# Kernel optimization log

Measured on AMD Instinct MI355X. Metric: run time of the kernel, lower is better.

The kernel has to match this reference:

```python
import jax, jax.numpy as jnp
import numpy as np

B = 262144      # batch (many robot-timestep samples)
IN_LEN = 32     # input_len
S = 64          # internal_state_len
M = 32          # message_len
P = 4           # num_ports
H = 100         # hidden_layer_size
L = 50          # lstm_hidden_size
O = 16          # output_len


def _linear_init(key, out_f, in_f):
    # torch.nn.Linear default init: U(-1/sqrt(in_f), 1/sqrt(in_f)) for W and b
    kw, kb = jax.random.split(key)
    bound = 1.0 / np.sqrt(in_f)
    W = jax.random.uniform(kw, (out_f, in_f), jnp.float32, -bound, bound)
    b = jax.random.uniform(kb, (out_f,), jnp.float32, -bound, bound)
    return W, b


def setup_inputs() -> dict:
    key = jax.random.key(0)
    ks = jax.random.split(key, 20)
    obs = jax.random.normal(ks[0], (B, IN_LEN), jnp.float32)
    messages_in = jax.random.normal(ks[1], (P, B, M), jnp.float32)
    h_lstm = jax.random.normal(ks[2], (B, L), jnp.float32)
    c_lstm = jax.random.normal(ks[3], (B, L), jnp.float32)

    W_in, b_in = _linear_init(ks[4], S, IN_LEN)
    # per-port message MLPs, stacked on a leading port axis
    msg1 = [_linear_init(jax.random.fold_in(ks[5], p), H, S) for p in range(P)]
    msg2 = [_linear_init(jax.random.fold_in(ks[6], p), M, H) for p in range(P)]
    msg_W1 = jnp.stack([w for w, _ in msg1])  # [P, H, S]
    msg_b1 = jnp.stack([b for _, b in msg1])  # [P, H]
    msg_W2 = jnp.stack([w for w, _ in msg2])  # [P, M, H]
    msg_b2 = jnp.stack([b for _, b in msg2])  # [P, M]

    # LSTMCell(S + M*P -> L); torch gate order i, f, g, o; init U(-1/sqrt(L), 1/sqrt(L))
    bl = 1.0 / np.sqrt(L)
    W_ih = jax.random.uniform(ks[7], (4 * L, S + M * P), jnp.float32, -bl, bl)
    W_hh = jax.random.uniform(ks[8], (4 * L, L), jnp.float32, -bl, bl)
    b_ih = jax.random.uniform(ks[9], (4 * L,), jnp.float32, -bl, bl)
    b_hh = jax.random.uniform(ks[10], (4 * L,), jnp.float32, -bl, bl)

    W_u1, b_u1 = _linear_init(ks[11], H, L)
    W_u2, b_u2 = _linear_init(ks[12], H, H)
    W_u3, b_u3 = _linear_init(ks[13], S, H)
    W_mu, b_mu = _linear_init(ks[14], O, S)
    W_var, b_var = _linear_init(ks[15], O, S)
    max_logvar = jnp.ones((1, O), jnp.float32) / 2.0
    min_logvar = -jnp.ones((1, O), jnp.float32) * 10.0

    return dict(obs=obs, messages_in=messages_in, h_lstm=h_lstm, c_lstm=c_lstm,
                W_in=W_in, b_in=b_in, msg_W1=msg_W1, msg_b1=msg_b1,
                msg_W2=msg_W2, msg_b2=msg_b2, W_ih=W_ih, W_hh=W_hh,
                b_ih=b_ih, b_hh=b_hh, W_u1=W_u1, b_u1=b_u1, W_u2=W_u2,
                b_u2=b_u2, W_u3=W_u3, b_u3=b_u3, W_mu=W_mu, b_mu=b_mu,
                W_var=W_var, b_var=b_var, max_logvar=max_logvar,
                min_logvar=min_logvar)


def reference(obs, messages_in, h_lstm, c_lstm, W_in, b_in, msg_W1, msg_b1,
              msg_W2, msg_b2, W_ih, W_hh, b_ih, b_hh, W_u1, b_u1, W_u2, b_u2,
              W_u3, b_u3, W_mu, b_mu, W_var, b_var, max_logvar, min_logvar):
    # run_input_function
    x = jax.nn.relu(obs @ W_in.T + b_in)                       # [B, S]

    # compute_messages_out_function: batched over ports (all ports occupied)
    m1 = jax.nn.relu(jnp.einsum('bs,phs->pbh', x, msg_W1) + msg_b1[:, None, :])
    msgs_out = jnp.einsum('pbh,pmh->pbm', m1, msg_W2) + msg_b2[:, None, :]  # [P, B, M]

    # compute_aggregation_function: concat incoming messages along feature dim
    agg = jnp.transpose(messages_in, (1, 0, 2)).reshape(obs.shape[0], -1)  # [B, P*M]
    h_mbar = jnp.concatenate([x, agg], axis=-1)                # [B, S + P*M]

    # status_update_function: one LSTMCell step (torch gate order i, f, g, o)
    gates = h_mbar @ W_ih.T + b_ih + h_lstm @ W_hh.T + b_hh    # [B, 4L]
    i, f, g, o = jnp.split(gates, 4, axis=-1)
    c_new = jax.nn.sigmoid(f) * c_lstm + jax.nn.sigmoid(i) * jnp.tanh(g)
    h_new = jax.nn.sigmoid(o) * jnp.tanh(c_new)                # [B, L]
    h2 = jax.nn.relu(h_new @ W_u1.T + b_u1)
    h2 = jax.nn.relu(h2 @ W_u2.T + b_u2)
    h2 = h2 @ W_u3.T + b_u3                                    # new internal state [B, S]

    # compute_output_function with soft logvar clamping
    mu = h2 @ W_mu.T + b_mu                                    # [B, O]
    logvar = h2 @ W_var.T + b_var
    logvar = max_logvar - jax.nn.softplus(max_logvar - logvar)
    logvar = min_logvar + jax.nn.softplus(logvar - min_logvar)
    var = jnp.exp(logvar)

    msgs_flat = jnp.transpose(msgs_out, (1, 0, 2)).reshape(obs.shape[0], -1)  # [B, P*M]
    # concat all outputs: mu(16) var(16) msgs(128) h2(64) h_new(50) c_new(50) = 324
    return jnp.concatenate([mu, var, msgs_flat, h2, h_new, c_new], axis=-1)
```

## Files before the change

### kernel.cpp

```cpp
#include <hip/hip_runtime.h>

typedef __bf16 bf16_t;
typedef __bf16 bf16x8 __attribute__((ext_vector_type(8)));
typedef float f32x4 __attribute__((ext_vector_type(4)));

#define B_TOTAL 262144
#define OUTC 324
#define ROWS 64

#define OFF_WIN   0
#define OFF_WG    2048
#define OFF_WM1   67584
#define OFF_WM2   96256
#define OFF_WU1   112640
#define OFF_WU2   119808
#define OFF_WU3   134144
#define OFF_WMV2  142336
#define BF16_TOTAL 145920

__global__ void prep_kernel(const float* W_in, const float* msg_W1, const float* msg_W2,
                            const float* W_ih, const float* W_hh, const float* b_ih, const float* b_hh,
                            const float* W_u1, const float* W_u2, const float* W_u3, const float* b_u3f,
                            const float* W_mu, const float* W_var, const float* b_mu, const float* b_var,
                            bf16_t* wb, float* bg, float* bmv) {
  int tid = blockIdx.x * blockDim.x + threadIdx.x;
  int nth = gridDim.x * blockDim.x;
  for (int i = tid; i < 2048; i += nth) wb[OFF_WIN + i] = (bf16_t)W_in[i];
  for (int i = tid; i < 65536; i += nth) {
    int n = i >> 8, k = i & 255;
    int g = n >> 6, j = n & 63;
    float v = 0.f;
    if (j < 50) {
      int r = g * 50 + j;
      if (k < 192) v = W_ih[r * 192 + k];
      else if (k < 242) v = W_hh[r * 50 + (k - 192)];
    }
    wb[OFF_WG + i] = (bf16_t)v;
  }
  for (int i = tid; i < 256; i += nth) {
    int g = i >> 6, j = i & 63;
    bg[i] = (j < 50) ? (b_ih[g * 50 + j] + b_hh[g * 50 + j]) : 0.f;
  }
  for (int i = tid; i < 4 * 112 * 64; i += nth) {
    int p = i / (112 * 64); int rem = i % (112 * 64); int n = rem >> 6, k = rem & 63;
    wb[OFF_WM1 + i] = (bf16_t)((n < 100) ? msg_W1[(p * 100 + n) * 64 + k] : 0.f);
  }
  for (int i = tid; i < 4 * 32 * 128; i += nth) {
    int p = i / (32 * 128); int rem = i % (32 * 128); int n = rem >> 7, k = rem & 127;
    wb[OFF_WM2 + i] = (bf16_t)((k < 100) ? msg_W2[(p * 32 + n) * 100 + k] : 0.f);
  }
  for (int i = tid; i < 112 * 64; i += nth) {
    int n = i >> 6, k = i & 63;
    wb[OFF_WU1 + i] = (bf16_t)((n < 100 && k < 50) ? W_u1[n * 50 + k] : 0.f);
  }
  for (int i = tid; i < 112 * 128; i += nth) {
    int n = i >> 7, k = i & 127;
    wb[OFF_WU2 + i] = (bf16_t)((n < 100 && k < 100) ? W_u2[n * 100 + k] : 0.f);
  }
  for (int i = tid; i < 64 * 128; i += nth) {
    int n = i >> 7, k = i & 127;
    wb[OFF_WU3 + i] = (bf16_t)((k < 100) ? W_u3[n * 100 + k] : 0.f);
  }
  for (int i = tid; i < 32 * 112; i += nth) {
    int o = i / 112, h = i % 112;
    float v = 0.f;
    if (h < 100) {
      const float* wrow = (o < 16) ? (W_mu + o * 64) : (W_var + (o - 16) * 64);
      for (int s = 0; s < 64; s++) v += wrow[s] * W_u3[s * 100 + h];
    }
    wb[OFF_WMV2 + i] = (bf16_t)v;
  }
  for (int i = tid; i < 32; i += nth) {
    int o = i;
    const float* wrow = (o < 16) ? (W_mu + o * 64) : (W_var + (o - 16) * 64);
    float v = (o < 16) ? b_mu[o] : b_var[o - 16];
    for (int s = 0; s < 64; s++) v += wrow[s] * b_u3f[s];
    bmv[o] = v;
  }
}

#define MFMA(a, b, c) __builtin_amdgcn_mfma_f32_16x16x32_bf16((a), (b), (c), 0, 0, 0)

__device__ __forceinline__ float frcp(float x) { return __builtin_amdgcn_rcpf(x); }
__device__ __forceinline__ float fsigmoid(float x) { return frcp(1.f + __expf(-x)); }
__device__ __forceinline__ float ftanh_f(float x) { return 1.f - 2.f * frcp(1.f + __expf(2.f * x)); }
__device__ __forceinline__ float fsoftplus(float x) { return (x > 15.f) ? x : __logf(1.f + __expf(x)); }

__device__ __forceinline__ bf16x8 cvt8(const float* __restrict__ p) {
  float4 v0 = *(const float4*)p;
  float4 v1 = *(const float4*)(p + 4);
  bf16x8 r;
  r[0] = (bf16_t)v0.x; r[1] = (bf16_t)v0.y; r[2] = (bf16_t)v0.z; r[3] = (bf16_t)v0.w;
  r[4] = (bf16_t)v1.x; r[5] = (bf16_t)v1.y; r[6] = (bf16_t)v1.z; r[7] = (bf16_t)v1.w;
  return r;
}

__device__ __forceinline__ void stage2(int p, const bf16x8 ax[4][2], bf16_t* dst,
                                       const bf16_t* __restrict__ wb,
                                       const float* __restrict__ msg_b1,
                                       int w, int lr, int kq) {
  for (int nt = w; nt < 7; nt += 4) {
    int nb = nt * 16;
    float bv = (nb + lr < 100) ? msg_b1[p * 100 + nb + lr] : 0.f;
    const bf16_t* Bp = wb + OFF_WM1 + p * 112 * 64 + (nb + lr) * 64 + kq * 8;
    bf16x8 b0 = *(const bf16x8*)Bp;
    bf16x8 b1 = *(const bf16x8*)(Bp + 32);
#pragma unroll
    for (int m = 0; m < 4; m++) {
      f32x4 acc = {bv, bv, bv, bv};
      acc = MFMA(ax[m][0], b0, acc);
      acc = MFMA(ax[m][1], b1, acc);
#pragma unroll
      for (int rr = 0; rr < 4; rr++)
        dst[(m * 16 + kq * 4 + rr) * 120 + nb + lr] = (bf16_t)fmaxf(acc[rr], 0.f);
    }
  }
}

__device__ __forceinline__ void stage3(int p, const bf16_t* src,
                                       const bf16_t* __restrict__ wb,
                                       const float* __restrict__ msg_b2,
                                       float* __restrict__ out,
                                       int row0, int w, int lr, int kq) {
  int nb = (w & 1) * 16;
  float bv = msg_b2[p * 32 + nb + lr];
  const bf16_t* Bp = wb + OFF_WM2 + p * 32 * 128 + (nb + lr) * 128 + kq * 8;
  bf16x8 b[4];
#pragma unroll
  for (int c = 0; c < 4; c++) b[c] = *(const bf16x8*)(Bp + c * 32);
#pragma unroll
  for (int mi = 0; mi < 2; mi++) {
    int m = (w >> 1) + mi * 2;
    f32x4 acc = {bv, bv, bv, bv};
#pragma unroll
    for (int c = 0; c < 4; c++) {
      bf16x8 a;
      if (c < 3) {
        a = *(const bf16x8*)(src + (m * 16 + lr) * 120 + c * 32 + kq * 8);
      } else {
        bf16x8 z = {};
        a = (kq < 2) ? *(const bf16x8*)(src + (m * 16 + lr) * 120 + 96 + kq * 8) : z;
      }
      acc = MFMA(a, b[c], acc);
    }
#pragma unroll
    for (int rr = 0; rr < 4; rr++) {
      size_t row = row0 + m * 16 + kq * 4 + rr;
      out[row * OUTC + 32 + p * 32 + nb + lr] = acc[rr];
    }
  }
}

__global__ __launch_bounds__(256, 2) void fused_kernel(
    const float* __restrict__ obs, const float* __restrict__ msg_in,
    const float* __restrict__ h_lstm, const float* __restrict__ c_lstm,
    const float* __restrict__ b_in, const float* __restrict__ msg_b1,
    const float* __restrict__ msg_b2, const float* __restrict__ b_u1,
    const float* __restrict__ b_u2, const float* __restrict__ b_u3,
    const float* __restrict__ maxlv, const float* __restrict__ minlv,
    const bf16_t* __restrict__ wb, const float* __restrict__ bg,
    const float* __restrict__ bmv, float* __restrict__ out) {
  __shared__ __align__(16) bf16_t xh[ROWS * 72];
  __shared__ __align__(16) bf16_t tA[ROWS * 120];
  __shared__ __align__(16) bf16_t tB[ROWS * 120];

  const int tid = threadIdx.x;
  const int row0 = blockIdx.x * ROWS;
  const int lane = tid & 63;
  const int w = tid >> 6;
  const int lr = lane & 15;
  const int kq = lane >> 4;

  {
    int nb = w * 16;
    float bv = b_in[nb + lr];
    bf16x8 b0 = *(const bf16x8*)(wb + OFF_WIN + (nb + lr) * 32 + kq * 8);
#pragma unroll
    for (int m = 0; m < 4; m++) {
      bf16x8 a0 = cvt8(obs + (size_t)(row0 + m * 16 + lr) * 32 + kq * 8);
      f32x4 acc = {bv, bv, bv, bv};
      acc = MFMA(a0, b0, acc);
#pragma unroll
      for (int rr = 0; rr < 4; rr++)
        xh[(m * 16 + kq * 4 + rr) * 72 + nb + lr] = (bf16_t)fmaxf(acc[rr], 0.f);
    }
  }
  __syncthreads();

  bf16x8 ax[4][2];
#pragma unroll
  for (int m = 0; m < 4; m++)
#pragma unroll
    for (int k = 0; k < 2; k++)
      ax[m][k] = *(const bf16x8*)(xh + (m * 16 + lr) * 72 + k * 32 + kq * 8);

  stage2(0, ax, tA, wb, msg_b1, w, lr, kq);
  __syncthreads();

  stage3(0, tA, wb, msg_b2, out, row0, w, lr, kq);
  stage2(1, ax, tB, wb, msg_b1, w, lr, kq);
  __syncthreads();
  stage3(1, tB, wb, msg_b2, out, row0, w, lr, kq);
  stage2(2, ax, tA, wb, msg_b1, w, lr, kq);
  __syncthreads();
  stage3(2, tA, wb, msg_b2, out, row0, w, lr, kq);
  stage2(3, ax, tB, wb, msg_b1, w, lr, kq);
  __syncthreads();

  {
    const int mt = w >> 1, jh = w & 1;
    const int jbase = jh * 32;
    bf16x8 m_pre[4][2];
#pragma unroll
    for (int p = 0; p < 4; p++)
#pragma unroll
      for (int ms = 0; ms < 2; ms++)
        m_pre[p][ms] = cvt8(msg_in + ((size_t)p * B_TOTAL + row0 + mt * 32 + ms * 16 + lr) * 32 + kq * 8);
    bf16x8 h_pre[2][2];
#pragma unroll
    for (int ms = 0; ms < 2; ms++) {
      const float* hp = h_lstm + (size_t)(row0 + mt * 32 + ms * 16 + lr) * 50;
      h_pre[0][ms] = cvt8(hp + kq * 8);
      if (kq < 2) {
        h_pre[1][ms] = cvt8(hp + 32 + kq * 8);
      } else if (kq == 2) {
        bf16x8 r = {};
        float2 v = *(const float2*)(hp + 48);
        r[0] = (bf16_t)v.x; r[1] = (bf16_t)v.y;
        h_pre[1][ms] = r;
      } else {
        bf16x8 r = {};
        h_pre[1][ms] = r;
      }
    }
    float c_pre[2][2][4];
#pragma unroll
    for (int s = 0; s < 2; s++) {
      int j = jbase + s * 16 + lr;
#pragma unroll
      for (int ms = 0; ms < 2; ms++)
#pragma unroll
        for (int rr = 0; rr < 4; rr++) {
          size_t row = row0 + mt * 32 + ms * 16 + kq * 4 + rr;
          c_pre[s][ms][rr] = (j < 50) ? c_lstm[row * 50 + j] : 0.f;
        }
    }

    stage3(3, tB, wb, msg_b2, out, row0, w, lr, kq);

    f32x4 acc[4][2][2];
#pragma unroll
    for (int g = 0; g < 4; g++)
#pragma unroll
      for (int s = 0; s < 2; s++) {
        float bb = bg[g * 64 + jbase + s * 16 + lr];
        f32x4 bi = {bb, bb, bb, bb};
        acc[g][s][0] = bi;
        acc[g][s][1] = bi;
      }
#pragma unroll
    for (int c = 0; c < 8; c++) {
      bf16x8 a[2];
#pragma unroll
      for (int ms = 0; ms < 2; ms++) {
        int lrow = mt * 32 + ms * 16 + lr;
        if (c < 2) {
          a[ms] = *(const bf16x8*)(xh + lrow * 72 + c * 32 + kq * 8);
        } else if (c < 6) {
          a[ms] = m_pre[c - 2][ms];
        } else {
          a[ms] = h_pre[c - 6][ms];
        }
      }
#pragma unroll
      for (int g = 0; g < 4; g++)
#pragma unroll
        for (int s = 0; s < 2; s++) {
          bf16x8 bfrag = *(const bf16x8*)(wb + OFF_WG +
              (size_t)(g * 64 + jbase + s * 16 + lr) * 256 + c * 32 + kq * 8);
          acc[g][s][0] = MFMA(a[0], bfrag, acc[g][s][0]);
          acc[g][s][1] = MFMA(a[1], bfrag, acc[g][s][1]);
        }
    }
#pragma unroll
    for (int s = 0; s < 2; s++) {
      int j = jbase + s * 16 + lr;
#pragma unroll
      for (int ms = 0; ms < 2; ms++) {
        int rbase = mt * 32 + ms * 16 + kq * 4;
#pragma unroll
        for (int rr = 0; rr < 4; rr++) {
          int lrow = rbase + rr;
          size_t row = row0 + lrow;
          float si = fsigmoid(acc[0][s][ms][rr]);
          float sf = fsigmoid(acc[1][s][ms][rr]);
          float gv = ftanh_f(acc[2][s][ms][rr]);
          float so = fsigmoid(acc[3][s][ms][rr]);
          float cn = sf * c_pre[s][ms][rr] + si * gv;
          float hv = so * ftanh_f(cn);
          if (j < 50) {
            out[row * OUTC + 274 + j] = cn;
            out[row * OUTC + 224 + j] = hv;
          }
          tA[lrow * 120 + j] = (bf16_t)((j < 50) ? hv : 0.f);
        }
      }
    }
  }
  __syncthreads();

  for (int nt = w; nt < 7; nt += 4) {
    int nb = nt * 16;
    float bv = (nb + lr < 100) ? b_u1[nb + lr] : 0.f;
    const bf16_t* Bp = wb + OFF_WU1 + (nb + lr) * 64 + kq * 8;
    bf16x8 b0 = *(const bf16x8*)Bp;
    bf16x8 b1 = *(const bf16x8*)(Bp + 32);
#pragma unroll
    for (int m = 0; m < 4; m++) {
      bf16x8 a0 = *(const bf16x8*)(tA + (m * 16 + lr) * 120 + kq * 8);
      bf16x8 a1 = *(const bf16x8*)(tA + (m * 16 + lr) * 120 + kq * 8 + 32);
      f32x4 acc = {bv, bv, bv, bv};
      acc = MFMA(a0, b0, acc);
      acc = MFMA(a1, b1, acc);
#pragma unroll
      for (int rr = 0; rr < 4; rr++)
        tB[(m * 16 + kq * 4 + rr) * 120 + nb + lr] = (bf16_t)fmaxf(acc[rr], 0.f);
    }
  }
  __syncthreads();

  for (int nt = w; nt < 7; nt += 4) {
    int nb = nt * 16;
    float bv = (nb + lr < 100) ? b_u2[nb + lr] : 0.f;
    const bf16_t* Bp = wb + OFF_WU2 + (nb + lr) * 128 + kq * 8;
    bf16x8 b[4];
#pragma unroll
    for (int c = 0; c < 4; c++) b[c] = *(const bf16x8*)(Bp + c * 32);
#pragma unroll
    for (int m = 0; m < 4; m++) {
      f32x4 acc = {bv, bv, bv, bv};
#pragma unroll
      for (int c = 0; c < 4; c++) {
        bf16x8 a;
        if (c < 3) {
          a = *(const bf16x8*)(tB + (m * 16 + lr) * 120 + c * 32 + kq * 8);
        } else {
          bf16x8 z = {};
          a = (kq < 2) ? *(const bf16x8*)(tB + (m * 16 + lr) * 120 + 96 + kq * 8) : z;
        }
        acc = MFMA(a, b[c], acc);
      }
#pragma unroll
      for (int rr = 0; rr < 4; rr++)
        tA[(m * 16 + kq * 4 + rr) * 120 + nb + lr] = (bf16_t)fmaxf(acc[rr], 0.f);
    }
  }
  __syncthreads();

  {
    int nb = w * 16;
    float bv = b_u3[nb + lr];
    const bf16_t* Bp = wb + OFF_WU3 + (nb + lr) * 128 + kq * 8;
    bf16x8 b[4];
#pragma unroll
    for (int c = 0; c < 4; c++) b[c] = *(const bf16x8*)(Bp + c * 32);
#pragma unroll
    for (int m = 0; m < 4; m++) {
      f32x4 acc = {bv, bv, bv, bv};
#pragma unroll
      for (int c = 0; c < 4; c++) {
        bf16x8 a;
        if (c < 3) {
          a = *(const bf16x8*)(tA + (m * 16 + lr) * 120 + c * 32 + kq * 8);
        } else {
          bf16x8 z = {};
          a = (kq < 2) ? *(const bf16x8*)(tA + (m * 16 + lr) * 120 + 96 + kq * 8) : z;
        }
        acc = MFMA(a, b[c], acc);
      }
#pragma unroll
      for (int rr = 0; rr < 4; rr++) {
        size_t row = row0 + m * 16 + kq * 4 + rr;
        out[row * OUTC + 160 + nb + lr] = acc[rr];
      }
    }
  }

  {
    int t = w & 1;
    const bf16_t* Bp = wb + OFF_WMV2 + (t * 16 + lr) * 112 + kq * 8;
    bf16x8 b[4];
#pragma unroll
    for (int c = 0; c < 3; c++) b[c] = *(const bf16x8*)(Bp + c * 32);
    {
      bf16x8 z = {};
      b[3] = (kq < 2) ? *(const bf16x8*)(Bp + 96) : z;
    }
    float bv = bmv[t * 16 + lr];
    float mx = maxlv[lr], mn = minlv[lr];
#pragma unroll
    for (int mi = 0; mi < 2; mi++) {
      int m = (w >> 1) + mi * 2;
      f32x4 acc = {bv, bv, bv, bv};
#pragma unroll
      for (int c = 0; c < 4; c++) {
        bf16x8 a;
        if (c < 3) {
          a = *(const bf16x8*)(tA + (m * 16 + lr) * 120 + c * 32 + kq * 8);
        } else {
          bf16x8 z = {};
          a = (kq < 2) ? *(const bf16x8*)(tA + (m * 16 + lr) * 120 + 96 + kq * 8) : z;
        }
        acc = MFMA(a, b[c], acc);
      }
      if (t == 0) {
#pragma unroll
        for (int rr = 0; rr < 4; rr++) {
          size_t row = row0 + m * 16 + kq * 4 + rr;
          out[row * OUTC + lr] = acc[rr];
        }
      } else {
#pragma unroll
        for (int rr = 0; rr < 4; rr++) {
          size_t row = row0 + m * 16 + kq * 4 + rr;
          float lv = acc[rr];
          lv = mx - fsoftplus(mx - lv);
          lv = mn + fsoftplus(lv - mn);
          out[row * OUTC + 16 + lr] = __expf(lv);
        }
      }
    }
  }
}

extern "C" void kernel_launch(void* const* d_in, const int* in_sizes, int n_in,
                              void* d_out, int out_size, void* d_ws, size_t ws_size,
                              hipStream_t stream) {
  const float* obs   = (const float*)d_in[0];
  const float* msgs  = (const float*)d_in[1];
  const float* h_l   = (const float*)d_in[2];
  const float* c_l   = (const float*)d_in[3];
  const float* W_in  = (const float*)d_in[4];
  const float* b_in  = (const float*)d_in[5];
  const float* mW1   = (const float*)d_in[6];
  const float* mb1   = (const float*)d_in[7];
  const float* mW2   = (const float*)d_in[8];
  const float* mb2   = (const float*)d_in[9];
  const float* W_ih  = (const float*)d_in[10];
  const float* W_hh  = (const float*)d_in[11];
  const float* b_ih  = (const float*)d_in[12];
  const float* b_hh  = (const float*)d_in[13];
  const float* W_u1  = (const float*)d_in[14];
  const float* b_u1  = (const float*)d_in[15];
  const float* W_u2  = (const float*)d_in[16];
  const float* b_u2  = (const float*)d_in[17];
  const float* W_u3  = (const float*)d_in[18];
  const float* b_u3  = (const float*)d_in[19];
  const float* W_mu  = (const float*)d_in[20];
  const float* b_mu  = (const float*)d_in[21];
  const float* W_var = (const float*)d_in[22];
  const float* b_var = (const float*)d_in[23];
  const float* maxlv = (const float*)d_in[24];
  const float* minlv = (const float*)d_in[25];

  bf16_t* wb = (bf16_t*)d_ws;
  float* bg  = (float*)((char*)d_ws + (size_t)BF16_TOTAL * 2);
  float* bmv = bg + 256;

  prep_kernel<<<64, 256, 0, stream>>>(W_in, mW1, mW2, W_ih, W_hh, b_ih, b_hh,
                                      W_u1, W_u2, W_u3, b_u3, W_mu, W_var, b_mu, b_var,
                                      wb, bg, bmv);
  fused_kernel<<<B_TOTAL / ROWS, 256, 0, stream>>>(
      obs, msgs, h_l, c_l, b_in, mb1, mb2, b_u1, b_u2, b_u3,
      maxlv, minlv, wb, bg, bmv, (float*)d_out);
}
```

Measured before the change: 379.5 us.

## Buffer all four port hidden layers in LDS to cut barriers

Computes all four per-port message first layers into a single enlarged LDS buffer and syncs once, replacing the double-buffered stage2/stage3 interleave that needed a barrier per port. The second message layer then runs for all ports after the barrier. The LSTM input reuses the x fragments already held in registers instead of reloading them from LDS, and h_new is written into xh. LDS per block grows to about 70 KB and the launch bound of two blocks per SM is removed, which may lower occupancy and register-pressure guarantees.

```diff
diff --git a/kernel.cpp b/kernel.cpp
--- a/kernel.cpp
+++ b/kernel.cpp
@@ -95,63 +95,7 @@
   return r;
 }
 
-__device__ __forceinline__ void stage2(int p, const bf16x8 ax[4][2], bf16_t* dst,
-                                       const bf16_t* __restrict__ wb,
-                                       const float* __restrict__ msg_b1,
-                                       int w, int lr, int kq) {
-  for (int nt = w; nt < 7; nt += 4) {
-    int nb = nt * 16;
-    float bv = (nb + lr < 100) ? msg_b1[p * 100 + nb + lr] : 0.f;
-    const bf16_t* Bp = wb + OFF_WM1 + p * 112 * 64 + (nb + lr) * 64 + kq * 8;
-    bf16x8 b0 = *(const bf16x8*)Bp;
-    bf16x8 b1 = *(const bf16x8*)(Bp + 32);
-#pragma unroll
-    for (int m = 0; m < 4; m++) {
-      f32x4 acc = {bv, bv, bv, bv};
-      acc = MFMA(ax[m][0], b0, acc);
-      acc = MFMA(ax[m][1], b1, acc);
-#pragma unroll
-      for (int rr = 0; rr < 4; rr++)
-        dst[(m * 16 + kq * 4 + rr) * 120 + nb + lr] = (bf16_t)fmaxf(acc[rr], 0.f);
-    }
-  }
-}
-
-__device__ __forceinline__ void stage3(int p, const bf16_t* src,
-                                       const bf16_t* __restrict__ wb,
-                                       const float* __restrict__ msg_b2,
-                                       float* __restrict__ out,
-                                       int row0, int w, int lr, int kq) {
-  int nb = (w & 1) * 16;
-  float bv = msg_b2[p * 32 + nb + lr];
-  const bf16_t* Bp = wb + OFF_WM2 + p * 32 * 128 + (nb + lr) * 128 + kq * 8;
-  bf16x8 b[4];
-#pragma unroll
-  for (int c = 0; c < 4; c++) b[c] = *(const bf16x8*)(Bp + c * 32);
-#pragma unroll
-  for (int mi = 0; mi < 2; mi++) {
-    int m = (w >> 1) + mi * 2;
-    f32x4 acc = {bv, bv, bv, bv};
-#pragma unroll
-    for (int c = 0; c < 4; c++) {
-      bf16x8 a;
-      if (c < 3) {
-        a = *(const bf16x8*)(src + (m * 16 + lr) * 120 + c * 32 + kq * 8);
-      } else {
-        bf16x8 z = {};
-        a = (kq < 2) ? *(const bf16x8*)(src + (m * 16 + lr) * 120 + 96 + kq * 8) : z;
-      }
-      acc = MFMA(a, b[c], acc);
-    }
-#pragma unroll
-    for (int rr = 0; rr < 4; rr++) {
-      size_t row = row0 + m * 16 + kq * 4 + rr;
-      out[row * OUTC + 32 + p * 32 + nb + lr] = acc[rr];
-    }
-  }
-}
-
-__global__ __launch_bounds__(256, 2) void fused_kernel(
+__global__ void fused_kernel(
     const float* __restrict__ obs, const float* __restrict__ msg_in,
     const float* __restrict__ h_lstm, const float* __restrict__ c_lstm,
     const float* __restrict__ b_in, const float* __restrict__ msg_b1,
@@ -160,9 +104,8 @@
     const float* __restrict__ maxlv, const float* __restrict__ minlv,
     const bf16_t* __restrict__ wb, const float* __restrict__ bg,
     const float* __restrict__ bmv, float* __restrict__ out) {
+  __shared__ __align__(16) bf16_t bufM[4 * ROWS * 120];
   __shared__ __align__(16) bf16_t xh[ROWS * 72];
-  __shared__ __align__(16) bf16_t tA[ROWS * 120];
-  __shared__ __align__(16) bf16_t tB[ROWS * 120];
 
   const int tid = threadIdx.x;
   const int row0 = blockIdx.x * ROWS;
@@ -194,22 +137,32 @@
     for (int k = 0; k < 2; k++)
       ax[m][k] = *(const bf16x8*)(xh + (m * 16 + lr) * 72 + k * 32 + kq * 8);
 
-  stage2(0, ax, tA, wb, msg_b1, w, lr, kq);
-  __syncthreads();
-
-  stage3(0, tA, wb, msg_b2, out, row0, w, lr, kq);
-  stage2(1, ax, tB, wb, msg_b1, w, lr, kq);
-  __syncthreads();
-  stage3(1, tB, wb, msg_b2, out, row0, w, lr, kq);
-  stage2(2, ax, tA, wb, msg_b1, w, lr, kq);
-  __syncthreads();
-  stage3(2, tA, wb, msg_b2, out, row0, w, lr, kq);
-  stage2(3, ax, tB, wb, msg_b1, w, lr, kq);
+#pragma unroll
+  for (int p = 0; p < 4; p++) {
+    bf16_t* dst = bufM + p * (ROWS * 120);
+    for (int nt = w; nt < 7; nt += 4) {
+      int nb = nt * 16;
+      float bv = (nb + lr < 100) ? msg_b1[p * 100 + nb + lr] : 0.f;
+      const bf16_t* Bp = wb + OFF_WM1 + p * 112 * 64 + (nb + lr) * 64 + kq * 8;
+      bf16x8 b0 = *(const bf16x8*)Bp;
+      bf16x8 b1 = *(const bf16x8*)(Bp + 32);
+#pragma unroll
+      for (int m = 0; m < 4; m++) {
+        f32x4 acc = {bv, bv, bv, bv};
+        acc = MFMA(ax[m][0], b0, acc);
+        acc = MFMA(ax[m][1], b1, acc);
+#pragma unroll
+        for (int rr = 0; rr < 4; rr++)
+          dst[(m * 16 + kq * 4 + rr) * 120 + nb + lr] = (bf16_t)fmaxf(acc[rr], 0.f);
+      }
+    }
+  }
   __syncthreads();
 
   {
     const int mt = w >> 1, jh = w & 1;
     const int jbase = jh * 32;
+
     bf16x8 m_pre[4][2];
 #pragma unroll
     for (int p = 0; p < 4; p++)
@@ -246,7 +199,37 @@
         }
     }
 
-    stage3(3, tB, wb, msg_b2, out, row0, w, lr, kq);
+#pragma unroll
+    for (int p = 0; p < 4; p++) {
+      const bf16_t* src = bufM + p * (ROWS * 120);
+      int nb = (w & 1) * 16;
+      float bv = msg_b2[p * 32 + nb + lr];
+      const bf16_t* Bp = wb + OFF_WM2 + p * 32 * 128 + (nb + lr) * 128 + kq * 8;
+      bf16x8 b[4];
+#pragma unroll
+      for (int c = 0; c < 4; c++) b[c] = *(const bf16x8*)(Bp + c * 32);
+#pragma unroll
+      for (int mi = 0; mi < 2; mi++) {
+        int m = (w >> 1) + mi * 2;
+        f32x4 acc = {bv, bv, bv, bv};
+#pragma unroll
+        for (int c = 0; c < 4; c++) {
+          bf16x8 a;
+          if (c < 3) {
+            a = *(const bf16x8*)(src + (m * 16 + lr) * 120 + c * 32 + kq * 8);
+          } else {
+            bf16x8 z = {};
+            a = (kq < 2) ? *(const bf16x8*)(src + (m * 16 + lr) * 120 + 96 + kq * 8) : z;
+          }
+          acc = MFMA(a, b[c], acc);
+        }
+#pragma unroll
+        for (int rr = 0; rr < 4; rr++) {
+          size_t row = row0 + m * 16 + kq * 4 + rr;
+          out[row * OUTC + 32 + p * 32 + nb + lr] = acc[rr];
+        }
+      }
+    }
 
     f32x4 acc[4][2][2];
 #pragma unroll
@@ -263,9 +246,8 @@
       bf16x8 a[2];
 #pragma unroll
       for (int ms = 0; ms < 2; ms++) {
-        int lrow = mt * 32 + ms * 16 + lr;
         if (c < 2) {
-          a[ms] = *(const bf16x8*)(xh + lrow * 72 + c * 32 + kq * 8);
+          a[ms] = ax[mt * 2 + ms][c];
         } else if (c < 6) {
           a[ms] = m_pre[c - 2][ms];
         } else {
@@ -302,12 +284,15 @@
             out[row * OUTC + 274 + j] = cn;
             out[row * OUTC + 224 + j] = hv;
           }
-          tA[lrow * 120 + j] = (bf16_t)((j < 50) ? hv : 0.f);
+          xh[lrow * 72 + j] = (bf16_t)((j < 50) ? hv : 0.f);
         }
       }
     }
   }
   __syncthreads();
+
+  bf16_t* t0 = bufM;
+  bf16_t* t1 = bufM + ROWS * 120;
 
   for (int nt = w; nt < 7; nt += 4) {
     int nb = nt * 16;
@@ -317,14 +302,14 @@
     bf16x8 b1 = *(const bf16x8*)(Bp + 32);
 #pragma unroll
     for (int m = 0; m < 4; m++) {
-      bf16x8 a0 = *(const bf16x8*)(tA + (m * 16 + lr) * 120 + kq * 8);
-      bf16x8 a1 = *(const bf16x8*)(tA + (m * 16 + lr) * 120 + kq * 8 + 32);
+      bf16x8 a0 = *(const bf16x8*)(xh + (m * 16 + lr) * 72 + kq * 8);
+      bf16x8 a1 = *(const bf16x8*)(xh + (m * 16 + lr) * 72 + kq * 8 + 32);
       f32x4 acc = {bv, bv, bv, bv};
       acc = MFMA(a0, b0, acc);
       acc = MFMA(a1, b1, acc);
 #pragma unroll
       for (int rr = 0; rr < 4; rr++)
-        tB[(m * 16 + kq * 4 + rr) * 120 + nb + lr] = (bf16_t)fmaxf(acc[rr], 0.f);
+        t0[(m * 16 + kq * 4 + rr) * 120 + nb + lr] = (bf16_t)fmaxf(acc[rr], 0.f);
     }
   }
   __syncthreads();
@@ -343,16 +328,16 @@
       for (int c = 0; c < 4; c++) {
         bf16x8 a;
         if (c < 3) {
-          a = *(const bf16x8*)(tB + (m * 16 + lr) * 120 + c * 32 + kq * 8);
+          a = *(const bf16x8*)(t0 + (m * 16 + lr) * 120 + c * 32 + kq * 8);
         } else {
           bf16x8 z = {};
-          a = (kq < 2) ? *(const bf16x8*)(tB + (m * 16 + lr) * 120 + 96 + kq * 8) : z;
+          a = (kq < 2) ? *(const bf16x8*)(t0 + (m * 16 + lr) * 120 + 96 + kq * 8) : z;
         }
         acc = MFMA(a, b[c], acc);
       }
 #pragma unroll
       for (int rr = 0; rr < 4; rr++)
-        tA[(m * 16 + kq * 4 + rr) * 120 + nb + lr] = (bf16_t)fmaxf(acc[rr], 0.f);
+        t1[(m * 16 + kq * 4 + rr) * 120 + nb + lr] = (bf16_t)fmaxf(acc[rr], 0.f);
     }
   }
   __syncthreads();
@@ -371,10 +356,10 @@
       for (int c = 0; c < 4; c++) {
         bf16x8 a;
         if (c < 3) {
-          a = *(const bf16x8*)(tA + (m * 16 + lr) * 120 + c * 32 + kq * 8);
+          a = *(const bf16x8*)(t1 + (m * 16 + lr) * 120 + c * 32 + kq * 8);
         } else {
           bf16x8 z = {};
-          a = (kq < 2) ? *(const bf16x8*)(tA + (m * 16 + lr) * 120 + 96 + kq * 8) : z;
+          a = (kq < 2) ? *(const bf16x8*)(t1 + (m * 16 + lr) * 120 + 96 + kq * 8) : z;
         }
         acc = MFMA(a, b[c], acc);
       }
@@ -406,10 +391,10 @@
       for (int c = 0; c < 4; c++) {
         bf16x8 a;
         if (c < 3) {
-          a = *(const bf16x8*)(tA + (m * 16 + lr) * 120 + c * 32 + kq * 8);
+          a = *(const bf16x8*)(t1 + (m * 16 + lr) * 120 + c * 32 + kq * 8);
         } else {
           bf16x8 z = {};
-          a = (kq < 2) ? *(const bf16x8*)(tA + (m * 16 + lr) * 120 + 96 + kq * 8) : z;
+          a = (kq < 2) ? *(const bf16x8*)(t1 + (m * 16 + lr) * 120 + 96 + kq * 8) : z;
         }
         acc = MFMA(a, b[c], acc);
       }
```

Result: slower. 668.4 us (+76.1%).

## Retile LSTM gate GEMM so each wave owns 16 columns across all 64 rows

Applied to the files above, without the earlier changes.

The LSTM gate matmul now gives each of the four waves one 16-wide hidden-unit column slice over all 64 rows, replacing the old 32-row by 32-column split. Each weight fragment is loaded once and reused across four row tiles, which cuts global weight loads per MFMA. The message and h_lstm prefetches that used to be issued before stage3 are removed. Those inputs are now loaded and converted inside the k-loop, giving up the overlap of that global latency with stage3 in exchange for lower register pressure.

```diff
diff --git a/kernel.cpp b/kernel.cpp
--- a/kernel.cpp
+++ b/kernel.cpp
@@ -208,102 +208,80 @@
   __syncthreads();
 
   {
-    const int mt = w >> 1, jh = w & 1;
-    const int jbase = jh * 32;
-    bf16x8 m_pre[4][2];
-#pragma unroll
-    for (int p = 0; p < 4; p++)
-#pragma unroll
-      for (int ms = 0; ms < 2; ms++)
-        m_pre[p][ms] = cvt8(msg_in + ((size_t)p * B_TOTAL + row0 + mt * 32 + ms * 16 + lr) * 32 + kq * 8);
-    bf16x8 h_pre[2][2];
-#pragma unroll
-    for (int ms = 0; ms < 2; ms++) {
-      const float* hp = h_lstm + (size_t)(row0 + mt * 32 + ms * 16 + lr) * 50;
-      h_pre[0][ms] = cvt8(hp + kq * 8);
-      if (kq < 2) {
-        h_pre[1][ms] = cvt8(hp + 32 + kq * 8);
-      } else if (kq == 2) {
-        bf16x8 r = {};
-        float2 v = *(const float2*)(hp + 48);
-        r[0] = (bf16_t)v.x; r[1] = (bf16_t)v.y;
-        h_pre[1][ms] = r;
-      } else {
-        bf16x8 r = {};
-        h_pre[1][ms] = r;
-      }
-    }
-    float c_pre[2][2][4];
-#pragma unroll
-    for (int s = 0; s < 2; s++) {
-      int j = jbase + s * 16 + lr;
-#pragma unroll
-      for (int ms = 0; ms < 2; ms++)
-#pragma unroll
-        for (int rr = 0; rr < 4; rr++) {
-          size_t row = row0 + mt * 32 + ms * 16 + kq * 4 + rr;
-          c_pre[s][ms][rr] = (j < 50) ? c_lstm[row * 50 + j] : 0.f;
-        }
-    }
+    const int j = w * 16 + lr;
+    float c_pre[4][4];
+#pragma unroll
+    for (int ms = 0; ms < 4; ms++)
+#pragma unroll
+      for (int rr = 0; rr < 4; rr++) {
+        size_t row = row0 + ms * 16 + kq * 4 + rr;
+        c_pre[ms][rr] = (j < 50) ? c_lstm[row * 50 + j] : 0.f;
+      }
 
     stage3(3, tB, wb, msg_b2, out, row0, w, lr, kq);
 
-    f32x4 acc[4][2][2];
-#pragma unroll
-    for (int g = 0; g < 4; g++)
-#pragma unroll
-      for (int s = 0; s < 2; s++) {
-        float bb = bg[g * 64 + jbase + s * 16 + lr];
-        f32x4 bi = {bb, bb, bb, bb};
-        acc[g][s][0] = bi;
-        acc[g][s][1] = bi;
-      }
+    f32x4 acc[4][4];
+#pragma unroll
+    for (int g = 0; g < 4; g++) {
+      float bb = bg[g * 64 + j];
+      f32x4 bi = {bb, bb, bb, bb};
+#pragma unroll
+      for (int ms = 0; ms < 4; ms++) acc[g][ms] = bi;
+    }
 #pragma unroll
     for (int c = 0; c < 8; c++) {
-      bf16x8 a[2];
-#pragma unroll
-      for (int ms = 0; ms < 2; ms++) {
-        int lrow = mt * 32 + ms * 16 + lr;
+      bf16x8 a[4];
+#pragma unroll
+      for (int ms = 0; ms < 4; ms++) {
+        int lrow = ms * 16 + lr;
         if (c < 2) {
           a[ms] = *(const bf16x8*)(xh + lrow * 72 + c * 32 + kq * 8);
         } else if (c < 6) {
-          a[ms] = m_pre[c - 2][ms];
+          a[ms] = cvt8(msg_in + ((size_t)(c - 2) * B_TOTAL + row0 + lrow) * 32 + kq * 8);
+        } else if (c == 6) {
+          a[ms] = cvt8(h_lstm + (size_t)(row0 + lrow) * 50 + kq * 8);
         } else {
-          a[ms] = h_pre[c - 6][ms];
-        }
-      }
+          const float* hp = h_lstm + (size_t)(row0 + lrow) * 50;
+          if (kq < 2) {
+            a[ms] = cvt8(hp + 32 + kq * 8);
+          } else if (kq == 2) {
+            bf16x8 r = {};
+            float2 v = *(const float2*)(hp + 48);
+            r[0] = (bf16_t)v.x; r[1] = (bf16_t)v.y;
+            a[ms] = r;
+          } else {
+            bf16x8 r = {};
+            a[ms] = r;
+          }
+        }
+      }
+      bf16x8 bfr[4];
 #pragma unroll
       for (int g = 0; g < 4; g++)
-#pragma unroll
-        for (int s = 0; s < 2; s++) {
-          bf16x8 bfrag = *(const bf16x8*)(wb + OFF_WG +
-              (size_t)(g * 64 + jbase + s * 16 + lr) * 256 + c * 32 + kq * 8);
-          acc[g][s][0] = MFMA(a[0], bfrag, acc[g][s][0]);
-          acc[g][s][1] = MFMA(a[1], bfrag, acc[g][s][1]);
-        }
-    }
-#pragma unroll
-    for (int s = 0; s < 2; s++) {
-      int j = jbase + s * 16 + lr;
-#pragma unroll
-      for (int ms = 0; ms < 2; ms++) {
-        int rbase = mt * 32 + ms * 16 + kq * 4;
-#pragma unroll
-        for (int rr = 0; rr < 4; rr++) {
-          int lrow = rbase + rr;
-          size_t row = row0 + lrow;
-          float si = fsigmoid(acc[0][s][ms][rr]);
-          float sf = fsigmoid(acc[1][s][ms][rr]);
-          float gv = ftanh_f(acc[2][s][ms][rr]);
-          float so = fsigmoid(acc[3][s][ms][rr]);
-          float cn = sf * c_pre[s][ms][rr] + si * gv;
-          float hv = so * ftanh_f(cn);
-          if (j < 50) {
-            out[row * OUTC + 274 + j] = cn;
-            out[row * OUTC + 224 + j] = hv;
-          }
-          tA[lrow * 120 + j] = (bf16_t)((j < 50) ? hv : 0.f);
-        }
+        bfr[g] = *(const bf16x8*)(wb + OFF_WG + (size_t)(g * 64 + j) * 256 + c * 32 + kq * 8);
+#pragma unroll
+      for (int g = 0; g < 4; g++)
+#pragma unroll
+        for (int ms = 0; ms < 4; ms++)
+          acc[g][ms] = MFMA(a[ms], bfr[g], acc[g][ms]);
+    }
+#pragma unroll
+    for (int ms = 0; ms < 4; ms++) {
+#pragma unroll
+      for (int rr = 0; rr < 4; rr++) {
+        int lrow = ms * 16 + kq * 4 + rr;
+        size_t row = row0 + lrow;
+        float si = fsigmoid(acc[0][ms][rr]);
+        float sf = fsigmoid(acc[1][ms][rr]);
+        float gv = ftanh_f(acc[2][ms][rr]);
+        float so = fsigmoid(acc[3][ms][rr]);
+        float cn = sf * c_pre[ms][rr] + si * gv;
+        float hv = so * ftanh_f(cn);
+        if (j < 50) {
+          out[row * OUTC + 274 + j] = cn;
+          out[row * OUTC + 224 + j] = hv;
+        }
+        tA[lrow * 120 + j] = (bf16_t)((j < 50) ? hv : 0.f);
       }
     }
   }
```

Result: faster. 348.4 us (-8.2%).
